# Kernel optimization log

Measured on AMD Instinct MI355X. Metric: run time of the kernel, lower is better.

The kernel has to match this reference:

```python
import jax, jax.numpy as jnp
import numpy as np

B, S, A, H, E = 8192, 256, 64, 1024, 8
IN = S + A
OUT = S + 1


def setup_inputs() -> dict:
    key = jax.random.key(0)
    ks = jax.random.split(key, 8)
    state = jax.random.normal(ks[0], (B, S), dtype=jnp.float32)
    action = jax.random.normal(ks[1], (B, A), dtype=jnp.float32)
    idx = jax.random.randint(ks[2], (B,), 0, E, dtype=jnp.int32)
    # Kaiming-ish scaling to keep activations sane
    W1 = jax.random.normal(ks[3], (E, IN, H), dtype=jnp.float32) / np.sqrt(IN)
    b1 = jnp.zeros((E, H), dtype=jnp.float32)
    W2 = jax.random.normal(ks[4], (E, H, H), dtype=jnp.float32) / np.sqrt(H)
    b2 = jnp.zeros((E, H), dtype=jnp.float32)
    W3 = jax.random.normal(ks[5], (E, H, OUT), dtype=jnp.float32) / np.sqrt(H)
    b3 = jnp.zeros((E, OUT), dtype=jnp.float32)
    return {"state": state, "action": action, "idx": idx,
            "W1": W1, "b1": b1, "W2": W2, "b2": b2, "W3": W3, "b3": b3}


def reference(state, action, idx, W1, b1, W2, b2, W3, b3):
    # Dense-MoE style: run all E experts on the full batch, then select the
    # per-sample expert output chosen by idx (matches masked gather/scatter
    # in the torch predict loop).
    x = jnp.concatenate([state, action], axis=-1)                  # [B, IN]
    h = jax.nn.relu(jnp.einsum('bi,eih->beh', x, W1) + b1)         # [B, E, H]
    h = jax.nn.relu(jnp.einsum('beh,ehk->bek', h, W2) + b2)        # [B, E, H]
    out = jnp.einsum('beh,eho->beo', h, W3) + b3                   # [B, E, S+1]
    sel = jnp.take_along_axis(out, idx[:, None, None], axis=1)[:, 0]  # [B, S+1]
    s_dim = state.shape[-1]
    delta = sel[:, :s_dim]
    reward = sel[:, s_dim:]
    next_state = state + delta
    return next_state, reward
```

## Files before the change

### kernel.cpp

```cpp
#include <hip/hip_runtime.h>
#include <stdint.h>

#define B_SZ   8192
#define IN_DIM 320
#define H_DIM  1024
#define E_NUM  8
#define OUT_DIM 257
#define TM     64
#define MAXT   (B_SZ / TM + E_NUM)
#define W3ROWS 320
#define NG12   (MAXT * 16)
#define NG3    (MAXT * 5)
#define NAUX   2568

typedef __bf16 bf16x8 __attribute__((ext_vector_type(8)));
typedef float  f32x4  __attribute__((ext_vector_type(4)));

typedef unsigned int __attribute__((address_space(1))) as1_uint;
typedef unsigned int __attribute__((address_space(3))) as3_uint;

__device__ __forceinline__ void gload_lds16(const void* g, void* l) {
    __builtin_amdgcn_global_load_lds((const as1_uint*)g, (as3_uint*)l, 16, 0, 0);
}

__device__ __forceinline__ unsigned short f2bf(float f) {
    unsigned int u = __float_as_uint(f);
    return (unsigned short)((u + 0x7fffu + ((u >> 16) & 1u)) >> 16);
}

__device__ __forceinline__ void trans64(const float* __restrict__ src,
                                        unsigned short* __restrict__ dst,
                                        int Ks, int Ns, int dR, int e, int kt,
                                        int nt, unsigned short* sh,
                                        int tid, int nthr) {
    int k0 = kt * 64, n0 = nt * 64;
    const float* s = src + (size_t)e * Ks * Ns + (size_t)k0 * Ns + n0;
    unsigned short* d = dst + ((size_t)e * dR + n0) * Ks + k0;
    int tx = tid & 63, wv = tid >> 6, nw = nthr >> 6;
    for (int rr = wv; rr < 64; rr += nw)
        sh[rr * 66 + tx] = f2bf(s[(size_t)rr * Ns + tx]);
    __syncthreads();
    int kq = tid & 15, nr = (tid >> 4) & 3;
    for (int p = 0; p < 16 / nw; p++) {
        int n = (wv + p * nw) * 4 + nr;
        ushort4 o;
        o.x = sh[(kq * 4 + 0) * 66 + n];
        o.y = sh[(kq * 4 + 1) * 66 + n];
        o.z = sh[(kq * 4 + 2) * 66 + n];
        o.w = sh[(kq * 4 + 3) * 66 + n];
        *(ushort4*)&d[(size_t)n * Ks + kq * 4] = o;
    }
}

__global__ __launch_bounds__(256)
void k_prep0(const float* __restrict__ state, const float* __restrict__ action,
             const int* __restrict__ idx, const float* __restrict__ W1,
             unsigned short* __restrict__ xb, unsigned short* __restrict__ w1t,
             int* __restrict__ order, int* __restrict__ te,
             int* __restrict__ tp0, int* __restrict__ tcnt) {
    __shared__ unsigned short sh[64 * 66];
    __shared__ int scnt[16][E_NUM];
    int bid = blockIdx.x, tid = threadIdx.x;

    if (bid == 0) {
        int shard = tid & 15;
        if (tid < 128) ((int*)scnt)[tid] = 0;
        __syncthreads();
        for (int b = tid; b < B_SZ; b += 256) atomicAdd(&scnt[shard][idx[b]], 1);
        __syncthreads();
        if (tid == 0) {
            int pos = 0, tt = 0;
            for (int e = 0; e < E_NUM; e++) {
                int start = pos;
                for (int s = 0; s < 16; s++) { int c = scnt[s][e]; scnt[s][e] = pos; pos += c; }
                int tot = pos - start;
                for (int st = 0; st < tot; st += TM) {
                    te[tt] = e; tp0[tt] = start + st; tcnt[tt] = min(TM, tot - st); tt++;
                }
            }
            for (; tt < MAXT; tt++) { te[tt] = 0; tp0[tt] = 0; tcnt[tt] = 0; }
        }
        __syncthreads();
        for (int b = tid; b < B_SZ; b += 256) {
            int e = idx[b];
            int p = atomicAdd(&scnt[shard][e], 1);
            order[p] = b;
        }
        return;
    }

    if (bid <= 320) {
        int a = bid - 1;
        const float4* sf = (const float4*)state;
        const float4* af = (const float4*)action;
#pragma unroll
        for (int p = 0; p < 8; p++) {
            int q = a * 2048 + p * 256 + tid;
            int b = q / 80, j = q % 80;
            float4 v = (j < 64) ? sf[b * 64 + j] : af[b * 16 + (j - 64)];
            ushort4 o;
            o.x = f2bf(v.x); o.y = f2bf(v.y); o.z = f2bf(v.z); o.w = f2bf(v.w);
            ((ushort4*)xb)[q] = o;
        }
        return;
    }

    int c = bid - 321;
    int e = c / 80, m = c % 80, kt = m / 16, nt = m % 16;
    trans64(W1, w1t, IN_DIM, H_DIM, H_DIM, e, kt, nt, sh, tid, 256);
}

template <int K, bool GATHER, int MODE, bool AUX>
__global__ __launch_bounds__(64, 2)
void k_gemm(const unsigned short* __restrict__ Abase,
            const unsigned short* __restrict__ Wt, int wtRows,
            const float* __restrict__ bias, int bstride,
            unsigned short* __restrict__ Hout,
            float* __restrict__ Out, const float* __restrict__ state,
            const int* __restrict__ order,
            const int* __restrict__ te, const int* __restrict__ tp0,
            const int* __restrict__ tcnt, int ng,
            const float* __restrict__ W2, unsigned short* __restrict__ w2t,
            const float* __restrict__ W3, unsigned short* __restrict__ w3t) {
    __shared__ __align__(16) char lds[16384];
    int bid = blockIdx.x, lane = threadIdx.x;

    if (AUX && bid >= ng) {
        int a = bid - ng;
        if (a < 2048) {
            trans64(W2, w2t, H_DIM, H_DIM, H_DIM, a >> 8, (a & 255) >> 4, a & 15,
                    (unsigned short*)lds, lane, 64);
        } else if (a < 2560) {
            int b = a - 2048;
            trans64(W3, w3t, H_DIM, OUT_DIM, W3ROWS, b >> 6, (b & 63) >> 2, b & 3,
                    (unsigned short*)lds, lane, 64);
        } else {
            int e = a - 2560;
#pragma unroll
            for (int p = 0; p < 16; p++) {
                int k = p * 64 + lane;
                w3t[((size_t)e * W3ROWS + 256) * H_DIM + k] =
                    f2bf(W3[((size_t)e * H_DIM + k) * OUT_DIM + 256]);
            }
        }
        return;
    }

    int t = bid % MAXT, ny = bid / MAXT;
    int cnt = tcnt[t];
    if (cnt == 0) return;
    int e = te[t], p0 = tp0[t];
    int n0 = ny * 64;
    constexpr int NI = K / 32;

    int r  = lane >> 2;
    int cg = (lane & 3) ^ ((r >> 1) & 3);
    const unsigned short* aP[4];
    const unsigned short* bP[4];
#pragma unroll
    for (int g = 0; g < 4; g++) {
        int rm = g * 16 + r;
        int rc = rm < cnt ? rm : cnt - 1;
        long ar = GATHER ? order[p0 + rc] : (p0 + rc);
        aP[g] = Abase + (size_t)ar * K + cg * 8;
        bP[g] = Wt + ((size_t)e * wtRows + n0 + rm) * K + cg * 8;
    }
    auto stage = [&](int k0, int sb) {
#pragma unroll
        for (int g = 0; g < 4; g++) {
            gload_lds16(aP[g] + k0, lds + sb + g * 1024 + lane * 16);
            gload_lds16(bP[g] + k0, lds + sb + 4096 + g * 1024 + lane * 16);
        }
    };

    f32x4 acc[4][4];
#pragma unroll
    for (int i = 0; i < 4; i++)
#pragma unroll
        for (int j = 0; j < 4; j++) acc[i][j] = (f32x4)0.f;

    const int fm   = lane & 15;
    const int koff = ((lane >> 4) ^ ((fm >> 1) & 3)) * 8;

    stage(0, 0);
    for (int it = 0; it < NI; ++it) {
        __syncthreads();
        if (it + 1 < NI) stage((it + 1) * 32, ((it + 1) & 1) * 8192);
        const unsigned short* As = (const unsigned short*)(lds + (it & 1) * 8192);
        const unsigned short* Bs = As + 2048;

        bf16x8 af[4], bf[4];
#pragma unroll
        for (int i = 0; i < 4; i++)
            af[i] = *(const bf16x8*)&As[(i * 16 + fm) * 32 + koff];
#pragma unroll
        for (int j = 0; j < 4; j++)
            bf[j] = *(const bf16x8*)&Bs[(j * 16 + fm) * 32 + koff];
#pragma unroll
        for (int i = 0; i < 4; i++)
#pragma unroll
            for (int j = 0; j < 4; j++)
                acc[i][j] = __builtin_amdgcn_mfma_f32_16x16x32_bf16(
                    af[i], bf[j], acc[i][j], 0, 0, 0);
    }

    int col = lane & 15, rq = lane >> 4;
#pragma unroll
    for (int j = 0; j < 4; j++) {
        int n = n0 + j * 16 + col;
        float bv = (MODE == 0) ? bias[e * bstride + n]
                               : ((n <= 256) ? bias[e * bstride + n] : 0.f);
#pragma unroll
        for (int i = 0; i < 4; i++) {
#pragma unroll
            for (int rr = 0; rr < 4; rr++) {
                int m = i * 16 + rq * 4 + rr;
                if (m < cnt) {
                    float v = acc[i][j][rr] + bv;
                    if (MODE == 0) {
                        Hout[(size_t)(p0 + m) * H_DIM + n] = f2bf(fmaxf(v, 0.f));
                    } else {
                        int row = order[p0 + m];
                        if (n < 256) {
                            size_t o = (size_t)row * 256 + n;
                            Out[o] = state[o] + v;
                        } else if (n == 256) {
                            Out[(size_t)B_SZ * 256 + row] = v;
                        }
                    }
                }
            }
        }
    }
}

extern "C" void kernel_launch(void* const* d_in, const int* in_sizes, int n_in,
                              void* d_out, int out_size, void* d_ws, size_t ws_size,
                              hipStream_t stream) {
    const float* state  = (const float*)d_in[0];
    const float* action = (const float*)d_in[1];
    const int*   idx    = (const int*)d_in[2];
    const float* W1     = (const float*)d_in[3];
    const float* b1     = (const float*)d_in[4];
    const float* W2     = (const float*)d_in[5];
    const float* b2     = (const float*)d_in[6];
    const float* W3     = (const float*)d_in[7];
    const float* b3     = (const float*)d_in[8];
    float* out = (float*)d_out;

    char* ws = (char*)d_ws;
    size_t off = 0;
    auto alloc = [&](size_t bytes) -> void* {
        void* p = ws + off;
        off = (off + bytes + 255) & ~(size_t)255;
        return p;
    };
    unsigned short* xb  = (unsigned short*)alloc((size_t)B_SZ * IN_DIM * 2);
    unsigned short* w1t = (unsigned short*)alloc((size_t)E_NUM * H_DIM * IN_DIM * 2);
    unsigned short* w2t = (unsigned short*)alloc((size_t)E_NUM * H_DIM * H_DIM * 2);
    unsigned short* w3t = (unsigned short*)alloc((size_t)E_NUM * W3ROWS * H_DIM * 2);
    unsigned short* h1  = (unsigned short*)alloc((size_t)B_SZ * H_DIM * 2);
    unsigned short* h2  = (unsigned short*)alloc((size_t)B_SZ * H_DIM * 2);
    int* order = (int*)alloc(B_SZ * 4);
    int* te    = (int*)alloc(MAXT * 4);
    int* tp0   = (int*)alloc(MAXT * 4);
    int* tcnt  = (int*)alloc(MAXT * 4);

    k_prep0<<<961, 256, 0, stream>>>(state, action, idx, W1, xb, w1t,
                                     order, te, tp0, tcnt);

    k_gemm<IN_DIM, true, 0, true><<<NG12 + NAUX, 64, 0, stream>>>(
        xb, w1t, H_DIM, b1, H_DIM, h1, nullptr, nullptr, order, te, tp0, tcnt,
        NG12, W2, w2t, W3, w3t);
    k_gemm<H_DIM, false, 0, false><<<NG12, 64, 0, stream>>>(
        h1, w2t, H_DIM, b2, H_DIM, h2, nullptr, nullptr, order, te, tp0, tcnt,
        NG12, nullptr, nullptr, nullptr, nullptr);
    k_gemm<H_DIM, false, 1, false><<<NG3, 64, 0, stream>>>(
        h2, w3t, W3ROWS, b3, OUT_DIM, nullptr, out, state, order, te, tp0, tcnt,
        NG3, nullptr, nullptr, nullptr, nullptr);
}
```

Measured before the change: 272.4 us.

## Load GEMM fragments directly from global memory and vectorize weight transpose reads

The MoE GEMM kernel drops its double-buffered LDS staging (global_load_lds plus barriers) and has each lane load its bf16x8 A and B MFMA fragments straight from global memory, with the K loop fully unrolled. The weight transpose helper is templated on thread count and reads float4 rows where the width allows. This is meant to remove LDS traffic and block synchronization, but it loses LDS data reuse and cross-iteration prefetch. Global loads become strided per lane, so performance depends on L1/L2 hit rates and how the compiler schedules the loads.

```diff
diff --git a/kernel.cpp b/kernel.cpp
--- a/kernel.cpp
+++ b/kernel.cpp
@@ -16,33 +16,35 @@
 typedef __bf16 bf16x8 __attribute__((ext_vector_type(8)));
 typedef float  f32x4  __attribute__((ext_vector_type(4)));
 
-typedef unsigned int __attribute__((address_space(1))) as1_uint;
-typedef unsigned int __attribute__((address_space(3))) as3_uint;
-
-__device__ __forceinline__ void gload_lds16(const void* g, void* l) {
-    __builtin_amdgcn_global_load_lds((const as1_uint*)g, (as3_uint*)l, 16, 0, 0);
-}
-
 __device__ __forceinline__ unsigned short f2bf(float f) {
     unsigned int u = __float_as_uint(f);
     return (unsigned short)((u + 0x7fffu + ((u >> 16) & 1u)) >> 16);
 }
 
+template <int NT, bool VEC>
 __device__ __forceinline__ void trans64(const float* __restrict__ src,
                                         unsigned short* __restrict__ dst,
                                         int Ks, int Ns, int dR, int e, int kt,
-                                        int nt, unsigned short* sh,
-                                        int tid, int nthr) {
+                                        int nt, unsigned short* sh, int tid) {
     int k0 = kt * 64, n0 = nt * 64;
     const float* s = src + (size_t)e * Ks * Ns + (size_t)k0 * Ns + n0;
     unsigned short* d = dst + ((size_t)e * dR + n0) * Ks + k0;
-    int tx = tid & 63, wv = tid >> 6, nw = nthr >> 6;
-    for (int rr = wv; rr < 64; rr += nw)
-        sh[rr * 66 + tx] = f2bf(s[(size_t)rr * Ns + tx]);
+    if (VEC) {
+        int c4 = tid & 15, r0 = tid >> 4;
+        for (int r = r0; r < 64; r += NT / 16) {
+            float4 v = *(const float4*)&s[(size_t)r * Ns + c4 * 4];
+            ushort4 o;
+            o.x = f2bf(v.x); o.y = f2bf(v.y); o.z = f2bf(v.z); o.w = f2bf(v.w);
+            *(ushort4*)&sh[r * 66 + c4 * 4] = o;
+        }
+    } else {
+        int tx = tid & 63;
+        for (int r = tid >> 6; r < 64; r += NT / 64)
+            sh[r * 66 + tx] = f2bf(s[(size_t)r * Ns + tx]);
+    }
     __syncthreads();
-    int kq = tid & 15, nr = (tid >> 4) & 3;
-    for (int p = 0; p < 16 / nw; p++) {
-        int n = (wv + p * nw) * 4 + nr;
+    int kq = tid & 15;
+    for (int n = tid >> 4; n < 64; n += NT / 16) {
         ushort4 o;
         o.x = sh[(kq * 4 + 0) * 66 + n];
         o.y = sh[(kq * 4 + 1) * 66 + n];
@@ -106,8 +108,8 @@
     }
 
     int c = bid - 321;
-    int e = c / 80, m = c % 80, kt = m / 16, nt = m % 16;
-    trans64(W1, w1t, IN_DIM, H_DIM, H_DIM, e, kt, nt, sh, tid, 256);
+    int e = c / 80, m = c % 80;
+    trans64<256, true>(W1, w1t, IN_DIM, H_DIM, H_DIM, e, m / 16, m % 16, sh, tid);
 }
 
 template <int K, bool GATHER, int MODE, bool AUX>
@@ -122,18 +124,18 @@
             const int* __restrict__ tcnt, int ng,
             const float* __restrict__ W2, unsigned short* __restrict__ w2t,
             const float* __restrict__ W3, unsigned short* __restrict__ w3t) {
-    __shared__ __align__(16) char lds[16384];
     int bid = blockIdx.x, lane = threadIdx.x;
 
     if (AUX && bid >= ng) {
+        __shared__ unsigned short sh[64 * 66];
         int a = bid - ng;
         if (a < 2048) {
-            trans64(W2, w2t, H_DIM, H_DIM, H_DIM, a >> 8, (a & 255) >> 4, a & 15,
-                    (unsigned short*)lds, lane, 64);
+            trans64<64, true>(W2, w2t, H_DIM, H_DIM, H_DIM, a >> 8,
+                              (a & 255) >> 4, a & 15, sh, lane);
         } else if (a < 2560) {
             int b = a - 2048;
-            trans64(W3, w3t, H_DIM, OUT_DIM, W3ROWS, b >> 6, (b & 63) >> 2, b & 3,
-                    (unsigned short*)lds, lane, 64);
+            trans64<64, false>(W3, w3t, H_DIM, OUT_DIM, W3ROWS, b >> 6,
+                               (b & 63) >> 2, b & 3, sh, lane);
         } else {
             int e = a - 2560;
 #pragma unroll
@@ -151,27 +153,19 @@
     if (cnt == 0) return;
     int e = te[t], p0 = tp0[t];
     int n0 = ny * 64;
-    constexpr int NI = K / 32;
-
-    int r  = lane >> 2;
-    int cg = (lane & 3) ^ ((r >> 1) & 3);
-    const unsigned short* aP[4];
-    const unsigned short* bP[4];
-#pragma unroll
-    for (int g = 0; g < 4; g++) {
-        int rm = g * 16 + r;
-        int rc = rm < cnt ? rm : cnt - 1;
-        long ar = GATHER ? order[p0 + rc] : (p0 + rc);
-        aP[g] = Abase + (size_t)ar * K + cg * 8;
-        bP[g] = Wt + ((size_t)e * wtRows + n0 + rm) * K + cg * 8;
-    }
-    auto stage = [&](int k0, int sb) {
-#pragma unroll
-        for (int g = 0; g < 4; g++) {
-            gload_lds16(aP[g] + k0, lds + sb + g * 1024 + lane * 16);
-            gload_lds16(bP[g] + k0, lds + sb + 4096 + g * 1024 + lane * 16);
-        }
-    };
+
+    const int fm = lane & 15;
+    const int kc = lane >> 4;
+
+    size_t arow[4];
+#pragma unroll
+    for (int i = 0; i < 4; i++) {
+        int m = i * 16 + fm;
+        int rc = m < cnt ? m : cnt - 1;
+        arow[i] = GATHER ? (size_t)order[p0 + rc] : (size_t)(p0 + rc);
+    }
+    const unsigned short* aB = Abase + kc * 8;
+    const unsigned short* bB = Wt + ((size_t)e * wtRows + n0 + fm) * K + kc * 8;
 
     f32x4 acc[4][4];
 #pragma unroll
@@ -179,23 +173,15 @@
 #pragma unroll
         for (int j = 0; j < 4; j++) acc[i][j] = (f32x4)0.f;
 
-    const int fm   = lane & 15;
-    const int koff = ((lane >> 4) ^ ((fm >> 1) & 3)) * 8;
-
-    stage(0, 0);
-    for (int it = 0; it < NI; ++it) {
-        __syncthreads();
-        if (it + 1 < NI) stage((it + 1) * 32, ((it + 1) & 1) * 8192);
-        const unsigned short* As = (const unsigned short*)(lds + (it & 1) * 8192);
-        const unsigned short* Bs = As + 2048;
-
+#pragma unroll
+    for (int k0 = 0; k0 < K; k0 += 32) {
         bf16x8 af[4], bf[4];
 #pragma unroll
         for (int i = 0; i < 4; i++)
-            af[i] = *(const bf16x8*)&As[(i * 16 + fm) * 32 + koff];
+            af[i] = *(const bf16x8*)(aB + arow[i] * K + k0);
 #pragma unroll
         for (int j = 0; j < 4; j++)
-            bf[j] = *(const bf16x8*)&Bs[(j * 16 + fm) * 32 + koff];
+            bf[j] = *(const bf16x8*)(bB + (size_t)j * 16 * K + k0);
 #pragma unroll
         for (int i = 0; i < 4; i++)
 #pragma unroll
```

After: 316.0 us. 16.0% more time.
